# Performance work log

Measured on AMD Instinct MI355X. Metric: run time of the kernel, lower is better.

Reference implementation:

```python
import jax, jax.numpy as jnp
import numpy as np

B = 8192
DV = 768   # visual_input_size
DT = 768   # text_input_size
E = 8      # num_experts
D = 1024   # expert_output_size
G = 2 * D  # gate_input_size
EPS = 1e-5


def setup_inputs() -> dict:
    key = jax.random.key(0)
    ks = jax.random.split(key, 14)
    s = lambda fan_in: 1.0 / np.sqrt(fan_in)
    return {
        "visual_features": jax.random.normal(ks[0], (B, DV), dtype=jnp.float32),
        "text_features": jax.random.normal(ks[1], (B, DT), dtype=jnp.float32),
        "vis_w": jax.random.uniform(ks[2], (DV, D), jnp.float32, -s(DV), s(DV)),
        "vis_b": jax.random.uniform(ks[3], (D,), jnp.float32, -s(DV), s(DV)),
        "txt_w": jax.random.uniform(ks[4], (DT, D), jnp.float32, -s(DT), s(DT)),
        "txt_b": jax.random.uniform(ks[5], (D,), jnp.float32, -s(DT), s(DT)),
        "gate_w": jax.random.uniform(ks[6], (G, E), jnp.float32, -s(G), s(G)),
        "gate_b": jax.random.uniform(ks[7], (E,), jnp.float32, -s(G), s(G)),
        "w1": jax.random.uniform(ks[8], (E, G, D), jnp.float32, -s(G), s(G)),
        "b1": jax.random.uniform(ks[9], (E, D), jnp.float32, -s(G), s(G)),
        "w2": jax.random.uniform(ks[10], (E, D, D), jnp.float32, -s(D), s(D)),
        "b2": jax.random.uniform(ks[11], (E, D), jnp.float32, -s(D), s(D)),
        "ln_g": jnp.ones((E, D), dtype=jnp.float32),
        "ln_b": jnp.zeros((E, D), dtype=jnp.float32),
    }


def reference(visual_features, text_features, vis_w, vis_b, txt_w, txt_b,
              gate_w, gate_b, w1, b1, w2, b2, ln_g, ln_b):
    # Projections + concat -> combined features [B, 2D]
    pv = visual_features @ vis_w + vis_b
    pt = text_features @ txt_w + txt_b
    combined = jnp.concatenate([pv, pt], axis=1)

    # Gate (dropout is identity at inference)
    gate_probs = jax.nn.softmax(combined @ gate_w + gate_b, axis=1)  # [B, E]

    # All experts as batched GEMMs: [B,G] x [E,G,D] -> [B,E,D]
    h = jnp.einsum('bg,egd->bed', combined, w1) + b1
    h = jax.nn.gelu(h, approximate=False)  # torch nn.GELU default = exact erf
    h = jnp.einsum('bed,edo->beo', h, w2) + b2

    # Per-expert LayerNorm over last dim
    mu = jnp.mean(h, axis=-1, keepdims=True)
    var = jnp.mean(jnp.square(h - mu), axis=-1, keepdims=True)
    h = (h - mu) * jax.lax.rsqrt(var + EPS) * ln_g + ln_b

    # Gated reduction over experts
    return jnp.einsum('bed,be->bd', h, gate_probs)
```

## Files before the change

kernel.cpp:

```cpp
#include <hip/hip_runtime.h>
#include <hip/hip_bf16.h>
#include <math.h>

#define BM 128
#define BN 128
#define BK 64

typedef __bf16 bf16x8_t __attribute__((ext_vector_type(8)));
typedef __bf16 bf16x4_t __attribute__((ext_vector_type(4)));
typedef float f32x16_t __attribute__((ext_vector_type(16)));

static __device__ __forceinline__ float bf2f(__bf16 b) {
    unsigned short s = __builtin_bit_cast(unsigned short, b);
    unsigned int u = ((unsigned int)s) << 16;
    return __builtin_bit_cast(float, u);
}
static __device__ __forceinline__ __bf16 f2bf(float f) {
    unsigned int u = __builtin_bit_cast(unsigned int, f);
    unsigned int r = (u + 0x7fffu + ((u >> 16) & 1u)) >> 16;
    return __builtin_bit_cast(__bf16, (unsigned short)r);
}
static __device__ __forceinline__ float gelu_fast(float x) {
    const float s = x * (0.7978845608f + 0.0356774081f * x * x);
    const float e = __expf(-2.0f * s);
    return x * __builtin_amdgcn_rcpf(1.0f + e);
}

#define GLDS16(gp, lp)                                                                   \
    __builtin_amdgcn_global_load_lds((const __attribute__((address_space(1))) void*)(gp), \
                                     (__attribute__((address_space(3))) void*)(lp), 16, 0, 0)

__global__ __launch_bounds__(256) void frag_cast(const float* __restrict__ in,
                                                 __bf16* __restrict__ out,
                                                 int K, int N,
                                                 size_t inStride, size_t outStride) {
    in += (size_t)blockIdx.z * inStride;
    out += (size_t)blockIdx.z * outStride;
    __shared__ float tile[64][65];
    const int k0 = blockIdx.x * 64, n0 = blockIdx.y * 64;
    const int tid = threadIdx.x;
    const int r = tid >> 4, c4 = (tid & 15) * 4;
#pragma unroll
    for (int p = 0; p < 4; ++p) {
        const float4 v = *(const float4*)&in[(size_t)(k0 + r + p * 16) * N + n0 + c4];
        tile[r + p * 16][c4 + 0] = v.x;
        tile[r + p * 16][c4 + 1] = v.y;
        tile[r + p * 16][c4 + 2] = v.z;
        tile[r + p * 16][c4 + 3] = v.w;
    }
    __syncthreads();
    const int c = tid >> 5, nn0 = (tid & 31) * 2;
#pragma unroll
    for (int t = 0; t < 2; ++t) {
        const int nn = nn0 + t;
        bf16x8_t v;
#pragma unroll
        for (int j = 0; j < 8; ++j) v[j] = f2bf(tile[c * 8 + j][nn]);
        *(bf16x8_t*)&out[((size_t)(k0 >> 3) + c) * N * 8 + (size_t)(n0 + nn) * 8] = v;
    }
}

__global__ __launch_bounds__(256) void cast_kernel(const float* __restrict__ in,
                                                   __bf16* __restrict__ out, int n8) {
    const int i = blockIdx.x * 256 + threadIdx.x;
    if (i < n8) {
        const float4* p = (const float4*)(in + (size_t)i * 8);
        const float4 a = p[0], b = p[1];
        bf16x8_t v;
        v[0] = f2bf(a.x); v[1] = f2bf(a.y); v[2] = f2bf(a.z); v[3] = f2bf(a.w);
        v[4] = f2bf(b.x); v[5] = f2bf(b.y); v[6] = f2bf(b.z); v[7] = f2bf(b.w);
        *(bf16x8_t*)(out + (size_t)i * 8) = v;
    }
}

template <int ACT>
__global__ __launch_bounds__(256) void gemm_bt(const __bf16* __restrict__ Ab, int lda, size_t strideAe,
                                               const __bf16* __restrict__ Bb, int Bn, size_t strideBe,
                                               const float* __restrict__ biasb, size_t strideBiasE,
                                               __bf16* __restrict__ Cb, int ldc, size_t strideCe,
                                               int K) {
    __shared__ __bf16 As[BM * BK];

    const __bf16* A = Ab + (size_t)blockIdx.z * strideAe;
    const __bf16* Bt = Bb + (size_t)blockIdx.z * strideBe;
    const float* bias = biasb + (size_t)blockIdx.z * strideBiasE;
    __bf16* C = Cb + (size_t)blockIdx.z * strideCe;

    const int tid = threadIdx.x;
    const int bm = blockIdx.x, bn = blockIdx.y;
    const int lane = tid & 63, wave = tid >> 6;
    const int wm = wave >> 1, wn = wave & 1;
    const int l = lane & 31, hi = lane >> 5;

    const int srow = tid >> 3;
    const int schunk = (tid & 7) ^ (srow & 7);
    const __bf16* ag = A + (size_t)(bm * BM + srow) * lda + schunk * 8;
    __bf16* asl = As + tid * 8;

    const int c0 = hi ^ (l & 7);
    const __bf16* base_a = As + (size_t)(wm * 64 + l) * BK;

    const size_t Bn8 = (size_t)Bn * 8;
    const __bf16* bbase = Bt + (size_t)hi * Bn8 + (size_t)(bn * BN + wn * 64 + l) * 8;

    f32x16_t acc[2][2] = {};

    const int nk = K / BK;
    for (int kt = 0; kt < nk; ++kt) {
        bf16x8_t bfr[4][2];
        const __bf16* bp = bbase + (size_t)(kt * 8) * Bn8;
#pragma unroll
        for (int s = 0; s < 4; ++s) {
            bfr[s][0] = *(const bf16x8_t*)(bp + (size_t)(2 * s) * Bn8);
            bfr[s][1] = *(const bf16x8_t*)(bp + (size_t)(2 * s) * Bn8 + 256);
        }
        GLDS16(ag, asl);
        GLDS16(ag + (size_t)32 * lda, asl + 2048);
        GLDS16(ag + (size_t)64 * lda, asl + 4096);
        GLDS16(ag + (size_t)96 * lda, asl + 6144);
        ag += BK;
        __syncthreads();
#pragma unroll
        for (int s = 0; s < 4; ++s) {
            const int co = (c0 ^ (2 * s)) * 8;
            const bf16x8_t a0 = *(const bf16x8_t*)(base_a + co);
            const bf16x8_t a1 = *(const bf16x8_t*)(base_a + 2048 + co);
            acc[0][0] = __builtin_amdgcn_mfma_f32_32x32x16_bf16(a0, bfr[s][0], acc[0][0], 0, 0, 0);
            acc[0][1] = __builtin_amdgcn_mfma_f32_32x32x16_bf16(a0, bfr[s][1], acc[0][1], 0, 0, 0);
            acc[1][0] = __builtin_amdgcn_mfma_f32_32x32x16_bf16(a1, bfr[s][0], acc[1][0], 0, 0, 0);
            acc[1][1] = __builtin_amdgcn_mfma_f32_32x32x16_bf16(a1, bfr[s][1], acc[1][1], 0, 0, 0);
        }
        __syncthreads();
    }

    const int colbase = bn * BN + wn * 64 + l;
    const int rowbase = bm * BM + wm * 64 + 4 * hi;
#pragma unroll
    for (int ni = 0; ni < 2; ++ni) {
        const int col = colbase + ni * 32;
        const float bv = bias[col];
#pragma unroll
        for (int mi = 0; mi < 2; ++mi) {
#pragma unroll
            for (int v = 0; v < 16; ++v) {
                const int row = rowbase + mi * 32 + (v & 3) + 8 * (v >> 2);
                float x = acc[mi][ni][v] + bv;
                if (ACT == 1) x = gelu_fast(x);
                C[(size_t)row * ldc + col] = f2bf(x);
            }
        }
    }
}

__global__ __launch_bounds__(256) void gate_kernel(const __bf16* __restrict__ comb,
                                                   const float* __restrict__ gw,
                                                   const float* __restrict__ gb,
                                                   float* __restrict__ gate) {
    const int b = blockIdx.x, tid = threadIdx.x;
    const int lane = tid & 63, wv = tid >> 6;
    const __bf16* row = comb + (size_t)b * 2048;
    float a[8] = {0, 0, 0, 0, 0, 0, 0, 0};
    for (int k = tid; k < 2048; k += 256) {
        const float c = bf2f(row[k]);
        const float4* g4 = (const float4*)(gw + (size_t)k * 8);
        const float4 x = g4[0], y = g4[1];
        a[0] += c * x.x; a[1] += c * x.y; a[2] += c * x.z; a[3] += c * x.w;
        a[4] += c * y.x; a[5] += c * y.y; a[6] += c * y.z; a[7] += c * y.w;
    }
#pragma unroll
    for (int j = 0; j < 8; ++j)
        for (int off = 32; off; off >>= 1) a[j] += __shfl_down(a[j], off, 64);
    __shared__ float red[4][8];
    if (lane == 0) {
#pragma unroll
        for (int j = 0; j < 8; ++j) red[wv][j] = a[j];
    }
    __syncthreads();
    if (tid == 0) {
        float l[8];
        float m = -1e30f;
        for (int j = 0; j < 8; ++j) {
            l[j] = red[0][j] + red[1][j] + red[2][j] + red[3][j] + gb[j];
            m = fmaxf(m, l[j]);
        }
        float s = 0.f;
        for (int j = 0; j < 8; ++j) { l[j] = expf(l[j] - m); s += l[j]; }
        const float inv = 1.0f / s;
        for (int j = 0; j < 8; ++j) gate[(size_t)b * 8 + j] = l[j] * inv;
    }
}

__global__ __launch_bounds__(256) void ln_out_kernel(const __bf16* __restrict__ h2,
                                                     const float* __restrict__ gate,
                                                     const float* __restrict__ lng,
                                                     const float* __restrict__ lnb,
                                                     float* __restrict__ out,
                                                     int Eg, int g0, int accum) {
    const int b = blockIdx.x;
    const int tid = threadIdx.x;
    const int lane = tid & 63, wv = tid >> 6;
    const int d0 = tid * 4;
    __shared__ float sS[4], sSS[4];
    float* orow = out + (size_t)b * 1024 + d0;
    float o0, o1, o2, o3;
    if (accum) {
        const float4 p = *(const float4*)orow;
        o0 = p.x; o1 = p.y; o2 = p.z; o3 = p.w;
    } else {
        o0 = o1 = o2 = o3 = 0.f;
    }
    for (int e = 0; e < Eg; ++e) {
        const __bf16* hp = h2 + ((size_t)e * 8192 + b) * 1024 + d0;
        const bf16x4_t hv = *(const bf16x4_t*)hp;
        const float v0 = bf2f(hv[0]), v1 = bf2f(hv[1]), v2 = bf2f(hv[2]), v3 = bf2f(hv[3]);
        float s = v0 + v1 + v2 + v3;
        float ss = v0 * v0 + v1 * v1 + v2 * v2 + v3 * v3;
        for (int off = 32; off; off >>= 1) {
            s += __shfl_down(s, off, 64);
            ss += __shfl_down(ss, off, 64);
        }
        if (lane == 0) { sS[wv] = s; sSS[wv] = ss; }
        __syncthreads();
        const float S = sS[0] + sS[1] + sS[2] + sS[3];
        const float SS = sSS[0] + sSS[1] + sSS[2] + sSS[3];
        __syncthreads();
        const float mu = S * (1.0f / 1024.0f);
        const float var = SS * (1.0f / 1024.0f) - mu * mu;
        const float rstd = rsqrtf(var + 1e-5f);
        const float w = gate[(size_t)b * 8 + g0 + e];
        const float4 gg = *(const float4*)(lng + (size_t)(g0 + e) * 1024 + d0);
        const float4 bb = *(const float4*)(lnb + (size_t)(g0 + e) * 1024 + d0);
        o0 += w * ((v0 - mu) * rstd * gg.x + bb.x);
        o1 += w * ((v1 - mu) * rstd * gg.y + bb.y);
        o2 += w * ((v2 - mu) * rstd * gg.z + bb.z);
        o3 += w * ((v3 - mu) * rstd * gg.w + bb.w);
    }
    *(float4*)orow = make_float4(o0, o1, o2, o3);
}

extern "C" void kernel_launch(void* const* d_in, const int* in_sizes, int n_in,
                              void* d_out, int out_size, void* d_ws, size_t ws_size,
                              hipStream_t stream) {
    (void)in_sizes; (void)n_in; (void)out_size;
    const float* visual = (const float*)d_in[0];
    const float* text   = (const float*)d_in[1];
    const float* vis_w  = (const float*)d_in[2];
    const float* vis_b  = (const float*)d_in[3];
    const float* txt_w  = (const float*)d_in[4];
    const float* txt_b  = (const float*)d_in[5];
    const float* gate_w = (const float*)d_in[6];
    const float* gate_b = (const float*)d_in[7];
    const float* w1     = (const float*)d_in[8];
    const float* b1     = (const float*)d_in[9];
    const float* w2     = (const float*)d_in[10];
    const float* b2     = (const float*)d_in[11];
    const float* ln_g   = (const float*)d_in[12];
    const float* ln_b   = (const float*)d_in[13];
    float* out = (float*)d_out;

    const size_t B = 8192, DV = 768, D = 1024, G = 2048, E = 8;

    char* ws = (char*)d_ws;
    size_t o = 0;
    auto alloc = [&](size_t bytes) { size_t r = o; o = (o + bytes + 255) & ~(size_t)255; return r; };
    const size_t off_viswt = alloc(DV * D * 2);
    const size_t off_txtwt = alloc(DV * D * 2);
    const size_t off_w1t   = alloc(E * G * D * 2);
    const size_t off_w2t   = alloc(E * D * D * 2);
    const size_t off_comb  = alloc(B * G * 2);
    const size_t off_gate  = alloc(B * E * 4);
    const size_t fixedEnd = o;
    const size_t inpBytes = 2 * B * DV * 2;

    int Eg = 1;
    {
        const int cand[4] = {8, 4, 2, 1};
        for (int c = 0; c < 4; ++c) {
            size_t h = (size_t)cand[c] * B * D * 2;
            size_t r1 = h > inpBytes ? h : inpBytes;
            r1 = (r1 + 255) & ~(size_t)255;
            const size_t need = fixedEnd + r1 + h;
            if (need <= ws_size || cand[c] == 1) { Eg = cand[c]; break; }
        }
    }
    const size_t h1bytes = (size_t)Eg * B * D * 2;
    size_t r1sz = h1bytes > inpBytes ? h1bytes : inpBytes;
    r1sz = (r1sz + 255) & ~(size_t)255;
    const size_t off_r1 = fixedEnd;
    const size_t off_h2 = off_r1 + r1sz;

    __bf16* viswt = (__bf16*)(ws + off_viswt);
    __bf16* txtwt = (__bf16*)(ws + off_txtwt);
    __bf16* w1t   = (__bf16*)(ws + off_w1t);
    __bf16* w2t   = (__bf16*)(ws + off_w2t);
    __bf16* comb  = (__bf16*)(ws + off_comb);
    float*  gate  = (float*)(ws + off_gate);
    __bf16* vis_bf = (__bf16*)(ws + off_r1);
    __bf16* txt_bf = vis_bf + B * DV;
    __bf16* h1    = (__bf16*)(ws + off_r1);
    __bf16* h2    = (__bf16*)(ws + off_h2);

    frag_cast<<<dim3(DV / 64, D / 64, 1), 256, 0, stream>>>(vis_w, viswt, (int)DV, (int)D, 0, 0);
    frag_cast<<<dim3(DV / 64, D / 64, 1), 256, 0, stream>>>(txt_w, txtwt, (int)DV, (int)D, 0, 0);
    frag_cast<<<dim3(G / 64, D / 64, E), 256, 0, stream>>>(w1, w1t, (int)G, (int)D, G * D, G * D);
    frag_cast<<<dim3(D / 64, D / 64, E), 256, 0, stream>>>(w2, w2t, (int)D, (int)D, D * D, D * D);

    const int n8 = (int)(B * DV / 8);
    cast_kernel<<<(n8 + 255) / 256, 256, 0, stream>>>(visual, vis_bf, n8);
    cast_kernel<<<(n8 + 255) / 256, 256, 0, stream>>>(text, txt_bf, n8);

    gemm_bt<0><<<dim3(B / BM, D / BN, 1), 256, 0, stream>>>(vis_bf, (int)DV, 0, viswt, (int)D, 0,
                                                            vis_b, 0, comb, (int)G, 0, (int)DV);
    gemm_bt<0><<<dim3(B / BM, D / BN, 1), 256, 0, stream>>>(txt_bf, (int)DV, 0, txtwt, (int)D, 0,
                                                            txt_b, 0, comb + D, (int)G, 0, (int)DV);

    gate_kernel<<<(int)B, 256, 0, stream>>>(comb, gate_w, gate_b, gate);

    const int ng = 8 / Eg;
    for (int g = 0; g < ng; ++g) {
        const int g0 = g * Eg;
        gemm_bt<1><<<dim3(B / BM, D / BN, Eg), 256, 0, stream>>>(
            comb, (int)G, 0, w1t + (size_t)g0 * G * D, (int)D, G * D,
            b1 + (size_t)g0 * D, D, h1, (int)D, B * D, (int)G);
        gemm_bt<0><<<dim3(B / BM, D / BN, Eg), 256, 0, stream>>>(
            h1, (int)D, B * D, w2t + (size_t)g0 * D * D, (int)D, D * D,
            b2 + (size_t)g0 * D, D, h2, (int)D, B * D, (int)D);
        ln_out_kernel<<<(int)B, 256, 0, stream>>>(h2, gate, ln_g, ln_b, out, Eg, g0, g > 0 ? 1 : 0);
    }
}
```

Measured before the change: 829.1 us.

## Double-buffer A tile in LDS and prefetch B fragments one k-step ahead

The GEMM main loop now uses two LDS buffers for the A tile and two register sets for the B fragments, so loads for the next k-tile are issued before the MFMA work on the current one. This is meant to hide global-to-LDS and global-to-register latency behind compute. It also sets launch_bounds to 2 blocks per CU, doubles LDS use, and adds register pressure. The loop assumes nk is even, and it unconditionally loads tile kt+1, which would read out of range for an odd tile count.

After: 865.8 us. +4.4%, slower.

```diff
diff --git a/kernel.cpp b/kernel.cpp
--- a/kernel.cpp
+++ b/kernel.cpp
@@ -74,12 +74,12 @@
 }
 
 template <int ACT>
-__global__ __launch_bounds__(256) void gemm_bt(const __bf16* __restrict__ Ab, int lda, size_t strideAe,
-                                               const __bf16* __restrict__ Bb, int Bn, size_t strideBe,
-                                               const float* __restrict__ biasb, size_t strideBiasE,
-                                               __bf16* __restrict__ Cb, int ldc, size_t strideCe,
-                                               int K) {
-    __shared__ __bf16 As[BM * BK];
+__global__ __launch_bounds__(256, 2) void gemm_bt(const __bf16* __restrict__ Ab, int lda, size_t strideAe,
+                                                  const __bf16* __restrict__ Bb, int Bn, size_t strideBe,
+                                                  const float* __restrict__ biasb, size_t strideBiasE,
+                                                  __bf16* __restrict__ Cb, int ldc, size_t strideCe,
+                                                  int K) {
+    __shared__ __bf16 As[2][BM * BK];
 
     const __bf16* A = Ab + (size_t)blockIdx.z * strideAe;
     const __bf16* Bt = Bb + (size_t)blockIdx.z * strideBe;
@@ -94,43 +94,63 @@
 
     const int srow = tid >> 3;
     const int schunk = (tid & 7) ^ (srow & 7);
-    const __bf16* ag = A + (size_t)(bm * BM + srow) * lda + schunk * 8;
-    __bf16* asl = As + tid * 8;
+    const __bf16* agb = A + (size_t)(bm * BM + srow) * lda + schunk * 8;
 
     const int c0 = hi ^ (l & 7);
-    const __bf16* base_a = As + (size_t)(wm * 64 + l) * BK;
+    const int abase = (wm * 64 + l) * BK;
 
     const size_t Bn8 = (size_t)Bn * 8;
     const __bf16* bbase = Bt + (size_t)hi * Bn8 + (size_t)(bn * BN + wn * 64 + l) * 8;
 
     f32x16_t acc[2][2] = {};
+    bf16x8_t bA[8], bB[8];
 
     const int nk = K / BK;
-    for (int kt = 0; kt < nk; ++kt) {
-        bf16x8_t bfr[4][2];
+
+    auto glds_tile = [&](int kt, int buf) {
+        const __bf16* a = agb + (size_t)kt * BK;
+        __bf16* dst = &As[buf][tid * 8];
+        GLDS16(a, dst);
+        GLDS16(a + (size_t)32 * lda, dst + 2048);
+        GLDS16(a + (size_t)64 * lda, dst + 4096);
+        GLDS16(a + (size_t)96 * lda, dst + 6144);
+    };
+    auto loadB = [&](int kt, bf16x8_t* d) {
         const __bf16* bp = bbase + (size_t)(kt * 8) * Bn8;
 #pragma unroll
         for (int s = 0; s < 4; ++s) {
-            bfr[s][0] = *(const bf16x8_t*)(bp + (size_t)(2 * s) * Bn8);
-            bfr[s][1] = *(const bf16x8_t*)(bp + (size_t)(2 * s) * Bn8 + 256);
-        }
-        GLDS16(ag, asl);
-        GLDS16(ag + (size_t)32 * lda, asl + 2048);
-        GLDS16(ag + (size_t)64 * lda, asl + 4096);
-        GLDS16(ag + (size_t)96 * lda, asl + 6144);
-        ag += BK;
-        __syncthreads();
+            d[s * 2 + 0] = *(const bf16x8_t*)(bp + (size_t)(2 * s) * Bn8);
+            d[s * 2 + 1] = *(const bf16x8_t*)(bp + (size_t)(2 * s) * Bn8 + 256);
+        }
+    };
+    auto compute = [&](int buf, const bf16x8_t* b) {
+        const __bf16* ba = &As[buf][abase];
 #pragma unroll
         for (int s = 0; s < 4; ++s) {
             const int co = (c0 ^ (2 * s)) * 8;
-            const bf16x8_t a0 = *(const bf16x8_t*)(base_a + co);
-            const bf16x8_t a1 = *(const bf16x8_t*)(base_a + 2048 + co);
-            acc[0][0] = __builtin_amdgcn_mfma_f32_32x32x16_bf16(a0, bfr[s][0], acc[0][0], 0, 0, 0);
-            acc[0][1] = __builtin_amdgcn_mfma_f32_32x32x16_bf16(a0, bfr[s][1], acc[0][1], 0, 0, 0);
-            acc[1][0] = __builtin_amdgcn_mfma_f32_32x32x16_bf16(a1, bfr[s][0], acc[1][0], 0, 0, 0);
-            acc[1][1] = __builtin_amdgcn_mfma_f32_32x32x16_bf16(a1, bfr[s][1], acc[1][1], 0, 0, 0);
-        }
+            const bf16x8_t a0 = *(const bf16x8_t*)(ba + co);
+            const bf16x8_t a1 = *(const bf16x8_t*)(ba + 2048 + co);
+            acc[0][0] = __builtin_amdgcn_mfma_f32_32x32x16_bf16(a0, b[s * 2 + 0], acc[0][0], 0, 0, 0);
+            acc[0][1] = __builtin_amdgcn_mfma_f32_32x32x16_bf16(a0, b[s * 2 + 1], acc[0][1], 0, 0, 0);
+            acc[1][0] = __builtin_amdgcn_mfma_f32_32x32x16_bf16(a1, b[s * 2 + 0], acc[1][0], 0, 0, 0);
+            acc[1][1] = __builtin_amdgcn_mfma_f32_32x32x16_bf16(a1, b[s * 2 + 1], acc[1][1], 0, 0, 0);
+        }
+    };
+
+    glds_tile(0, 0);
+    loadB(0, bA);
+
+    for (int kt = 0; kt < nk; kt += 2) {
         __syncthreads();
+        glds_tile(kt + 1, 1);
+        loadB(kt + 1, bB);
+        compute(0, bA);
+        __syncthreads();
+        if (kt + 2 < nk) {
+            glds_tile(kt + 2, 0);
+            loadB(kt + 2, bA);
+        }
+        compute(1, bB);
     }
 
     const int colbase = bn * BN + wn * 64 + l;
```

## Fold input projections into expert W1 and gate weights algebraically

Applied to the files above, without the earlier changes.

Pre-multiplies the visual/text projection weights into each expert's first-layer weights (and the gate weights), so the first expert GEMM runs directly on the concatenated raw inputs with K=1536 instead of K=2048, and the separate projection GEMMs and combined buffer are removed. Biases are folded into a new per-expert bias vector via a reduction kernel with atomics. This trades per-call weight premultiplication (8 experts of 768x1024x1024 GEMMs) for fewer FLOPs in the batch-sized GEMMs, and changes rounding since the premultiplied weights are rounded to bf16.

Result: faster. 769.1 us (-7.2%).

```diff
diff --git a/kernel.cpp b/kernel.cpp
--- a/kernel.cpp
+++ b/kernel.cpp
@@ -60,34 +60,47 @@
     }
 }
 
-__global__ __launch_bounds__(256) void cast_kernel(const float* __restrict__ in,
-                                                   __bf16* __restrict__ out, int n8) {
+__global__ __launch_bounds__(256) void cast2_kernel(const float* __restrict__ a,
+                                                    const float* __restrict__ b,
+                                                    __bf16* __restrict__ out, int n8each) {
     const int i = blockIdx.x * 256 + threadIdx.x;
-    if (i < n8) {
-        const float4* p = (const float4*)(in + (size_t)i * 8);
-        const float4 a = p[0], b = p[1];
+    if (i < 2 * n8each) {
+        const float* src = (i < n8each) ? a : b;
+        const size_t idx = (i < n8each) ? (size_t)i : (size_t)(i - n8each);
+        const float4* p = (const float4*)(src + idx * 8);
+        const float4 x = p[0], y = p[1];
         bf16x8_t v;
-        v[0] = f2bf(a.x); v[1] = f2bf(a.y); v[2] = f2bf(a.z); v[3] = f2bf(a.w);
-        v[4] = f2bf(b.x); v[5] = f2bf(b.y); v[6] = f2bf(b.z); v[7] = f2bf(b.w);
+        v[0] = f2bf(x.x); v[1] = f2bf(x.y); v[2] = f2bf(x.z); v[3] = f2bf(x.w);
+        v[4] = f2bf(y.x); v[5] = f2bf(y.y); v[6] = f2bf(y.z); v[7] = f2bf(y.w);
         *(bf16x8_t*)(out + (size_t)i * 8) = v;
     }
 }
 
-template <int ACT>
-__global__ __launch_bounds__(256) void gemm_bt(const __bf16* __restrict__ Ab, int lda, size_t strideAe,
-                                               const __bf16* __restrict__ Bb, int Bn, size_t strideBe,
-                                               const float* __restrict__ biasb, size_t strideBiasE,
-                                               __bf16* __restrict__ Cb, int ldc, size_t strideCe,
-                                               int K) {
-    __shared__ __bf16 As[BM * BK];
-
-    const __bf16* A = Ab + (size_t)blockIdx.z * strideAe;
-    const __bf16* Bt = Bb + (size_t)blockIdx.z * strideBe;
-    const float* bias = biasb + (size_t)blockIdx.z * strideBiasE;
-    __bf16* C = Cb + (size_t)blockIdx.z * strideCe;
-
+__global__ __launch_bounds__(256) void cast_acat(const float* __restrict__ vis,
+                                                 const float* __restrict__ txt,
+                                                 __bf16* __restrict__ out, int total8) {
+    const int i = blockIdx.x * 256 + threadIdx.x;
+    if (i < total8) {
+        const int r = i / 192;
+        const int c8 = i - r * 192;
+        const float* src = (c8 < 96) ? vis + (size_t)r * 768 + (size_t)c8 * 8
+                                     : txt + (size_t)r * 768 + (size_t)(c8 - 96) * 8;
+        const float4* p = (const float4*)src;
+        const float4 x = p[0], y = p[1];
+        bf16x8_t v;
+        v[0] = f2bf(x.x); v[1] = f2bf(x.y); v[2] = f2bf(x.z); v[3] = f2bf(x.w);
+        v[4] = f2bf(y.x); v[5] = f2bf(y.y); v[6] = f2bf(y.z); v[7] = f2bf(y.w);
+        *(bf16x8_t*)(out + (size_t)i * 8) = v;
+    }
+}
+
+template <int ACT, int PACK>
+static __device__ __forceinline__ void gemm_core(const __bf16* __restrict__ A, int lda,
+                                                 const __bf16* __restrict__ Bt, int Bn,
+                                                 const float* __restrict__ bias,
+                                                 __bf16* __restrict__ C, int ldc, int K,
+                                                 int bm, int bn, __bf16* As) {
     const int tid = threadIdx.x;
-    const int bm = blockIdx.x, bn = blockIdx.y;
     const int lane = tid & 63, wave = tid >> 6;
     const int wm = wave >> 1, wn = wave & 1;
     const int l = lane & 31, hi = lane >> 5;
@@ -138,7 +151,7 @@
 #pragma unroll
     for (int ni = 0; ni < 2; ++ni) {
         const int col = colbase + ni * 32;
-        const float bv = bias[col];
+        const float bv = PACK ? 0.0f : bias[col];
 #pragma unroll
         for (int mi = 0; mi < 2; ++mi) {
 #pragma unroll
@@ -146,26 +159,87 @@
                 const int row = rowbase + mi * 32 + (v & 3) + 8 * (v >> 2);
                 float x = acc[mi][ni][v] + bv;
                 if (ACT == 1) x = gelu_fast(x);
-                C[(size_t)row * ldc + col] = f2bf(x);
+                if (PACK) {
+                    C[((size_t)(row >> 3)) * (size_t)ldc * 8 + (size_t)col * 8 + (row & 7)] = f2bf(x);
+                } else {
+                    C[(size_t)row * ldc + col] = f2bf(x);
+                }
             }
         }
     }
 }
 
-__global__ __launch_bounds__(256) void gate_kernel(const __bf16* __restrict__ comb,
+template <int ACT>
+__global__ __launch_bounds__(256) void gemm_bt(const __bf16* __restrict__ Ab, int lda, size_t strideAe,
+                                               const __bf16* __restrict__ Bb, int Bn, size_t strideBe,
+                                               const float* __restrict__ biasb, size_t strideBiasE,
+                                               __bf16* __restrict__ Cb, int ldc, size_t strideCe,
+                                               int K) {
+    __shared__ __bf16 As[BM * BK];
+    gemm_core<ACT, 0>(Ab + (size_t)blockIdx.z * strideAe, lda,
+                      Bb + (size_t)blockIdx.z * strideBe, Bn,
+                      biasb + (size_t)blockIdx.z * strideBiasE,
+                      Cb + (size_t)blockIdx.z * strideCe, ldc, K,
+                      blockIdx.x, blockIdx.y, As);
+}
+
+__global__ __launch_bounds__(256) void gemm_premul(const __bf16* __restrict__ wbf,
+                                                   const __bf16* __restrict__ w1t,
+                                                   __bf16* __restrict__ w1cat) {
+    __shared__ __bf16 As[BM * BK];
+    const int e = blockIdx.z & 7, hf = blockIdx.z >> 3;
+    gemm_core<0, 1>(wbf + (size_t)hf * 768 * 1024, 1024,
+                    w1t + (size_t)e * 2048 * 1024 + (size_t)hf * 128 * 1024 * 8, 1024,
+                    nullptr,
+                    w1cat + (size_t)e * 1536 * 1024 + (size_t)hf * 96 * 1024 * 8, 1024, 1024,
+                    blockIdx.x, blockIdx.y, As);
+}
+
+__global__ __launch_bounds__(256) void bias1_kernel(const float* __restrict__ w1,
+                                                    const float* __restrict__ vis_b,
+                                                    const float* __restrict__ txt_b,
+                                                    const float* __restrict__ b1,
+                                                    float* __restrict__ b1t) {
+    const int n = blockIdx.x * 256 + threadIdx.x;
+    const int e = blockIdx.y;
+    const int d0 = blockIdx.z * 512;
+    float acc = (blockIdx.z == 0) ? b1[(size_t)e * 1024 + n] : 0.0f;
+#pragma unroll 4
+    for (int d = d0; d < d0 + 512; ++d) {
+        const float bv = (d < 1024) ? vis_b[d] : txt_b[d - 1024];
+        acc += bv * w1[((size_t)e * 2048 + d) * 1024 + n];
+    }
+    atomicAdd(&b1t[(size_t)e * 1024 + n], acc);
+}
+
+__global__ __launch_bounds__(256) void gcat_kernel(const float* __restrict__ vis_w,
+                                                   const float* __restrict__ txt_w,
+                                                   const float* __restrict__ vis_b,
+                                                   const float* __restrict__ txt_b,
                                                    const float* __restrict__ gw,
                                                    const float* __restrict__ gb,
-                                                   float* __restrict__ gate) {
-    const int b = blockIdx.x, tid = threadIdx.x;
+                                                   float* __restrict__ gcat) {
+    const int v = blockIdx.x, tid = threadIdx.x;
     const int lane = tid & 63, wv = tid >> 6;
-    const __bf16* row = comb + (size_t)b * 2048;
     float a[8] = {0, 0, 0, 0, 0, 0, 0, 0};
-    for (int k = tid; k < 2048; k += 256) {
-        const float c = bf2f(row[k]);
-        const float4* g4 = (const float4*)(gw + (size_t)k * 8);
-        const float4 x = g4[0], y = g4[1];
-        a[0] += c * x.x; a[1] += c * x.y; a[2] += c * x.z; a[3] += c * x.w;
-        a[4] += c * y.x; a[5] += c * y.y; a[6] += c * y.z; a[7] += c * y.w;
+    if (v < 1536) {
+        const float* wr = (v < 768) ? vis_w + (size_t)v * 1024 : txt_w + (size_t)(v - 768) * 1024;
+        const int dbase = (v < 768) ? 0 : 1024;
+        for (int d = tid; d < 1024; d += 256) {
+            const float c = wr[d];
+            const float4* g4 = (const float4*)(gw + (size_t)(dbase + d) * 8);
+            const float4 x = g4[0], y = g4[1];
+            a[0] += c * x.x; a[1] += c * x.y; a[2] += c * x.z; a[3] += c * x.w;
+            a[4] += c * y.x; a[5] += c * y.y; a[6] += c * y.z; a[7] += c * y.w;
+        }
+    } else {
+        for (int d = tid; d < 2048; d += 256) {
+            const float c = (d < 1024) ? vis_b[d] : txt_b[d - 1024];
+            const float4* g4 = (const float4*)(gw + (size_t)d * 8);
+            const float4 x = g4[0], y = g4[1];
+            a[0] += c * x.x; a[1] += c * x.y; a[2] += c * x.z; a[3] += c * x.w;
+            a[4] += c * y.x; a[5] += c * y.y; a[6] += c * y.z; a[7] += c * y.w;
+        }
     }
 #pragma unroll
     for (int j = 0; j < 8; ++j)
@@ -176,11 +250,42 @@
         for (int j = 0; j < 8; ++j) red[wv][j] = a[j];
     }
     __syncthreads();
+    if (tid < 8) {
+        float s = red[0][tid] + red[1][tid] + red[2][tid] + red[3][tid];
+        if (v == 1536) s += gb[tid];
+        gcat[(size_t)v * 8 + tid] = s;
+    }
+}
+
+__global__ __launch_bounds__(256) void gate_kernel(const __bf16* __restrict__ acat,
+                                                   const float* __restrict__ gcat,
+                                                   float* __restrict__ gate) {
+    const int b = blockIdx.x, tid = threadIdx.x;
+    const int lane = tid & 63, wv = tid >> 6;
+    const __bf16* row = acat + (size_t)b * 1536;
+    float a[8] = {0, 0, 0, 0, 0, 0, 0, 0};
+    for (int k = tid; k < 1536; k += 256) {
+        const float c = bf2f(row[k]);
+        const float4* g4 = (const float4*)(gcat + (size_t)k * 8);
+        const float4 x = g4[0], y = g4[1];
+        a[0] += c * x.x; a[1] += c * x.y; a[2] += c * x.z; a[3] += c * x.w;
+        a[4] += c * y.x; a[5] += c * y.y; a[6] += c * y.z; a[7] += c * y.w;
+    }
+#pragma unroll
+    for (int j = 0; j < 8; ++j)
+        for (int off = 32; off; off >>= 1) a[j] += __shfl_down(a[j], off, 64);
+    __shared__ float red[4][8];
+    if (lane == 0) {
+#pragma unroll
+        for (int j = 0; j < 8; ++j) red[wv][j] = a[j];
+    }
+    __syncthreads();
     if (tid == 0) {
+        const float* bg = gcat + 1536 * 8;
         float l[8];
         float m = -1e30f;
         for (int j = 0; j < 8; ++j) {
-            l[j] = red[0][j] + red[1][j] + red[2][j] + red[3][j] + gb[j];
+            l[j] = red[0][j] + red[1][j] + red[2][j] + red[3][j] + bg[j];
             m = fmaxf(m, l[j]);
         }
         float s = 0.f;
@@ -258,70 +363,64 @@
     const float* ln_b   = (const float*)d_in[13];
     float* out = (float*)d_out;
 
-    const size_t B = 8192, DV = 768, D = 1024, G = 2048, E = 8;
+    const size_t B = 8192, DV = 768, D = 1024, G = 2048, E = 8, KC = 1536;
 
     char* ws = (char*)d_ws;
     size_t o = 0;
     auto alloc = [&](size_t bytes) { size_t r = o; o = (o + bytes + 255) & ~(size_t)255; return r; };
-    const size_t off_viswt = alloc(DV * D * 2);
-    const size_t off_txtwt = alloc(DV * D * 2);
-    const size_t off_w1t   = alloc(E * G * D * 2);
+    const size_t off_wbf   = alloc(2 * DV * D * 2);
+    const size_t off_w1cat = alloc(E * KC * D * 2);
     const size_t off_w2t   = alloc(E * D * D * 2);
-    const size_t off_comb  = alloc(B * G * 2);
+    const size_t off_b1t   = alloc(E * D * 4);
+    const size_t off_gcat  = alloc((KC * E + E) * 4);
     const size_t off_gate  = alloc(B * E * 4);
+    const size_t off_acat  = alloc(B * KC * 2);
     const size_t fixedEnd = o;
-    const size_t inpBytes = 2 * B * DV * 2;
+    const size_t w1tBytes = E * G * D * 2;
 
     int Eg = 1;
     {
         const int cand[4] = {8, 4, 2, 1};
         for (int c = 0; c < 4; ++c) {
-            size_t h = (size_t)cand[c] * B * D * 2;
-            size_t r1 = h > inpBytes ? h : inpBytes;
-            r1 = (r1 + 255) & ~(size_t)255;
-            const size_t need = fixedEnd + r1 + h;
-            if (need <= ws_size || cand[c] == 1) { Eg = cand[c]; break; }
-        }
-    }
-    const size_t h1bytes = (size_t)Eg * B * D * 2;
-    size_t r1sz = h1bytes > inpBytes ? h1bytes : inpBytes;
-    r1sz = (r1sz + 255) & ~(size_t)255;
-    const size_t off_r1 = fixedEnd;
-    const size_t off_h2 = off_r1 + r1sz;
-
-    __bf16* viswt = (__bf16*)(ws + off_viswt);
-    __bf16* txtwt = (__bf16*)(ws + off_txtwt);
-    __bf16* w1t   = (__bf16*)(ws + off_w1t);
+            size_t h2b = 2 * (size_t)cand[c] * B * D * 2;
+            size_t dyn = h2b > w1tBytes ? h2b : w1tBytes;
+            if (fixedEnd + dyn <= ws_size || cand[c] == 1) { Eg = cand[c]; break; }
+        }
+    }
+
+    __bf16* wbf   = (__bf16*)(ws + off_wbf);
+    __bf16* w1cat = (__bf16*)(ws + off_w1cat);
     __bf16* w2t   = (__bf16*)(ws + off_w2t);
-    __bf16* comb  = (__bf16*)(ws + off_comb);
+    float*  b1t   = (float*)(ws + off_b1t);
+    float*  gcat  = (float*)(ws + off_gcat);
     float*  gate  = (float*)(ws + off_gate);
-    __bf16* vis_bf = (__bf16*)(ws + off_r1);
-    __bf16* txt_bf = vis_bf + B * DV;
-    __bf16* h1    = (__bf16*)(ws + off_r1);
-    __bf16* h2    = (__bf16*)(ws + off_h2);
-
-    frag_cast<<<dim3(DV / 64, D / 64, 1), 256, 0, stream>>>(vis_w, viswt, (int)DV, (int)D, 0, 0);
-    frag_cast<<<dim3(DV / 64, D / 64, 1), 256, 0, stream>>>(txt_w, txtwt, (int)DV, (int)D, 0, 0);
+    __bf16* acat  = (__bf16*)(ws + off_acat);
+    __bf16* w1t   = (__bf16*)(ws + fixedEnd);
+    __bf16* h1    = (__bf16*)(ws + fixedEnd);
+    __bf16* h2    = h1 + (size_t)Eg * B * D;
+
+    const int nw8 = (int)(DV * D / 8);
+    cast2_kernel<<<(2 * nw8 + 255) / 256, 256, 0, stream>>>(vis_w, txt_w, wbf, nw8);
+    const int na8 = (int)(B * KC / 8);
+    cast_acat<<<(na8 + 255) / 256, 256, 0, stream>>>(visual, text, acat, na8);
+
     frag_cast<<<dim3(G / 64, D / 64, E), 256, 0, stream>>>(w1, w1t, (int)G, (int)D, G * D, G * D);
     frag_cast<<<dim3(D / 64, D / 64, E), 256, 0, stream>>>(w2, w2t, (int)D, (int)D, D * D, D * D);
 
-    const int n8 = (int)(B * DV / 8);
-    cast_kernel<<<(n8 + 255) / 256, 256, 0, stream>>>(visual, vis_bf, n8);
-    cast_kernel<<<(n8 + 255) / 256, 256, 0, stream>>>(text, txt_bf, n8);
-
-    gemm_bt<0><<<dim3(B / BM, D / BN, 1), 256, 0, stream>>>(vis_bf, (int)DV, 0, viswt, (int)D, 0,
-                                                            vis_b, 0, comb, (int)G, 0, (int)DV);
-    gemm_bt<0><<<dim3(B / BM, D / BN, 1), 256, 0, stream>>>(txt_bf, (int)DV, 0, txtwt, (int)D, 0,
-                                                            txt_b, 0, comb + D, (int)G, 0, (int)DV);
-
-    gate_kernel<<<(int)B, 256, 0, stream>>>(comb, gate_w, gate_b, gate);
+    gemm_premul<<<dim3(768 / BM, D / BN, 16), 256, 0, stream>>>(wbf, w1t, w1cat);
+
+    hipMemsetAsync(b1t, 0, E * D * 4, stream);
+    bias1_kernel<<<dim3(4, 8, 4), 256, 0, stream>>>(w1, vis_b, txt_b, b1, b1t);
+    gcat_kernel<<<1537, 256, 0, stream>>>(vis_w, txt_w, vis_b, txt_b, gate_w, gate_b, gcat);
+
+    gate_kernel<<<(int)B, 256, 0, stream>>>(acat, gcat, gate);
 
     const int ng = 8 / Eg;
     for (int g = 0; g < ng; ++g) {
         const int g0 = g * Eg;
         gemm_bt<1><<<dim3(B / BM, D / BN, Eg), 256, 0, stream>>>(
-            comb, (int)G, 0, w1t + (size_t)g0 * G * D, (int)D, G * D,
-            b1 + (size_t)g0 * D, D, h1, (int)D, B * D, (int)G);
+            acat, (int)KC, 0, w1cat + (size_t)g0 * KC * D, (int)D, KC * D,
+            b1t + (size_t)g0 * D, D, h1, (int)D, B * D, (int)KC);
         gemm_bt<0><<<dim3(B / BM, D / BN, Eg), 256, 0, stream>>>(
             h1, (int)D, B * D, w2t + (size_t)g0 * D * D, (int)D, D * D,
             b2 + (size_t)g0 * D, D, h2, (int)D, B * D, (int)D);
```
